# Optimization experiments

Hardware: AMD Instinct MI355X
Metric: run time of the kernel (lower is better)

The kernel has to match this reference:

```python
import jax, jax.numpy as jnp
import numpy as np

B, S, H, L, HEADS, VOCAB, POS = 32, 240, 1024, 8, 16, 48, 240
D = H // HEADS


def setup_inputs() -> dict:
    key = jax.random.key(0)
    ks = jax.random.split(key, 20)
    p = lambda k, shape: jax.random.normal(k, shape, jnp.float32) * 0.02
    x = jax.random.normal(ks[0], (B, S, VOCAB), jnp.float32)
    lengths = jnp.sort(jax.random.randint(ks[1], (B,), 120, S + 1))[::-1]
    lengths = lengths.at[0].set(S)  # padded max length == S
    return {
        "x": x,
        "w_emb": p(ks[2], (VOCAB, H)),
        "p_emb": p(ks[3], (POS, H)),
        "Wq": p(ks[4], (L, H, H)), "bq": p(ks[5], (L, H)),
        "Wk": p(ks[6], (L, H, H)), "bk": p(ks[7], (L, H)),
        "Wv": p(ks[8], (L, H, H)), "bv": p(ks[9], (L, H)),
        "W1": p(ks[10], (L, H, H)), "b1": p(ks[11], (L, H)),
        "W2": p(ks[12], (L, H, H)), "b2": p(ks[13], (L, H)),
        "ln1_s": jnp.ones((L, H), jnp.float32), "ln1_b": jnp.zeros((L, H), jnp.float32),
        "ln2_s": jnp.ones((L, H), jnp.float32), "ln2_b": jnp.zeros((L, H), jnp.float32),
        "Wfc": p(ks[14], (H, 4)), "bfc": p(ks[15], (4,)),
        "lengths": lengths,
    }


def _ln(x, s, b):
    m = jnp.mean(x, -1, keepdims=True)
    v = jnp.mean((x - m) ** 2, -1, keepdims=True)
    return (x - m) / jnp.sqrt(v + 1e-5) * s + b


def reference(x, w_emb, p_emb, Wq, bq, Wk, bk, Wv, bv, W1, b1, W2, b2,
              ln1_s, ln1_b, ln2_s, ln2_b, Wfc, bfc, lengths):
    tokens = jnp.argmax(x, -1)                      # [B,S] argmax over feature dim (48)
    valid = jnp.arange(S)[None, :] < lengths[:, None]  # [B,S] query-row validity
    # pack/unpack zeros out embeddings at padded positions; pos-enc added everywhere
    z = w_emb[tokens] * valid[..., None].astype(jnp.float32) + p_emb[None, :S]
    causal = jnp.tril(jnp.ones((S, S), bool))
    scale = 1.0 / jnp.sqrt(jnp.float32(H))          # source divides by sqrt(hidden), not sqrt(d_head)
    for i in range(L):
        q = (z @ Wq[i] + bq[i]).reshape(B, S, HEADS, D)
        k = (z @ Wk[i] + bk[i]).reshape(B, S, HEADS, D)
        v = (z @ Wv[i] + bv[i]).reshape(B, S, HEADS, D)
        scores = jnp.einsum('bqhd,bkhd->bhqk', q, k) * scale
        scores = jnp.where(causal, scores, -jnp.inf)
        # softmax over causal keys; padded query rows are zeroed (torch NaN->0 path)
        atten = jax.nn.softmax(scores, -1) * valid[:, None, :, None].astype(jnp.float32)
        out = jnp.einsum('bhqk,bkhd->bqhd', atten, v).reshape(B, S, H)
        z1 = _ln(z + out, ln1_s[i], ln1_b[i])       # dropout off in eval
        ff = jax.nn.gelu(z1 @ W1[i] + b1[i], approximate=False) @ W2[i] + b2[i]
        z = _ln(z1 + ff, ln2_s[i], ln2_b[i])
    z2 = jnp.mean(z, axis=1)                        # mean-pool includes padded positions (faithful)
    return jax.nn.softmax(z2 @ Wfc + bfc, axis=-1)
```

## Files before the change

### kernel.cpp

```cpp
#include <hip/hip_runtime.h>
#include <hip/hip_bf16.h>

#define Bz 32
#define Sz 240
#define Hz 1024
#define Lz 8
#define NHEADS 16
#define NVOCAB 48
#define DHEAD 64
#define VT_STRIDE 264

typedef unsigned short u16;
typedef unsigned int u32;
typedef __attribute__((ext_vector_type(8))) short short8v;
typedef __attribute__((ext_vector_type(4))) float floatx4;

__device__ __forceinline__ int get_len(const int* __restrict__ L, int b) {
  return (L[1] == 0) ? L[2 * b] : L[b];
}
__device__ __forceinline__ u16 f2bf(float f) {
  u32 u = __float_as_uint(f);
  return (u16)((u + 0x7FFFu + ((u >> 16) & 1u)) >> 16);
}
__device__ __forceinline__ float bf2f(u16 s) {
  return __uint_as_float(((u32)s) << 16);
}
__device__ __forceinline__ void async_copy16(const u16* g, u16* l) {
  __builtin_amdgcn_global_load_lds(
      (const __attribute__((address_space(1))) u32*)g,
      (__attribute__((address_space(3))) u32*)l, 16, 0, 0);
}

__global__ __launch_bounds__(256) void embed_kernel(
    const float* __restrict__ x, const float* __restrict__ w_emb,
    const float* __restrict__ p_emb, const int* __restrict__ lengths,
    float* __restrict__ z, u16* __restrict__ z_bf) {
  int bs = blockIdx.x;
  int b = bs / Sz, s = bs % Sz;
  __shared__ int stok;
  if (threadIdx.x == 0) {
    const float* xr = x + (size_t)bs * NVOCAB;
    float best = xr[0]; int bi = 0;
    for (int j = 1; j < NVOCAB; ++j) {
      float v = xr[j];
      if (v > best) { best = v; bi = j; }
    }
    stok = bi;
  }
  __syncthreads();
  int tok = stok;
  float valid = (s < get_len(lengths, b)) ? 1.f : 0.f;
  const float* we = w_emb + (size_t)tok * Hz;
  const float* pe = p_emb + (size_t)s * Hz;
  size_t base = (size_t)bs * Hz;
  for (int h = threadIdx.x; h < Hz; h += blockDim.x) {
    float v = we[h] * valid + pe[h];
    z[base + h] = v;
    z_bf[base + h] = f2bf(v);
  }
}

__global__ __launch_bounds__(256) void bias_concat(
    const float* __restrict__ bq, const float* __restrict__ bk,
    const float* __restrict__ bv, float* __restrict__ dst) {
  int i = blockIdx.x * 256 + threadIdx.x;
  int l = i / 3072, c = i % 3072;
  float v = (c < 1024) ? bq[l * 1024 + c]
          : (c < 2048) ? bk[l * 1024 + c - 1024]
                       : bv[l * 1024 + c - 2048];
  dst[i] = v;
}

struct WconvArgs { const float* src[5]; u16* dst[5]; };
__global__ __launch_bounds__(256) void wconv5(WconvArgs a) {
  __shared__ u16 T[32][33];
  const float* W = a.src[blockIdx.z];
  u16* wt = a.dst[blockIdx.z];
  int bi = blockIdx.y, bj = blockIdx.x;
  int r = threadIdx.x >> 3, c4 = (threadIdx.x & 7) * 4;
  float4 w4 = *(const float4*)(W + (size_t)(bi * 32 + r) * Hz + bj * 32 + c4);
  T[r][c4 + 0] = f2bf(w4.x); T[r][c4 + 1] = f2bf(w4.y);
  T[r][c4 + 2] = f2bf(w4.z); T[r][c4 + 3] = f2bf(w4.w);
  __syncthreads();
  u32 lo = (u32)T[c4 + 0][r] | ((u32)T[c4 + 1][r] << 16);
  u32 hi = (u32)T[c4 + 2][r] | ((u32)T[c4 + 3][r] << 16);
  uint2 val; val.x = lo; val.y = hi;
  *(uint2*)(wt + (size_t)(bj * 32 + r) * Hz + bi * 32 + c4) = val;
}

template <int BN, bool OUTBF16, bool GELU, bool RESID>
__global__ __launch_bounds__(512, 2) void gemm_mfma(
    const u16* __restrict__ A, const u16* __restrict__ Wt,
    const float* __restrict__ bias, const float* __restrict__ resid,
    void* __restrict__ Cv, int nco) {
  constexpr int MT = (BN == 256) ? 8 : 4;
  constexpr int WGC = (BN == 256) ? 4 : 2;
  constexpr int BKT = BN * 32;
  __shared__ u16 As[2][16384];
  __shared__ u16 Bs[2][BN * 64];
  int tid = threadIdx.x;
  int nwg = (int)gridDim.x;
  int id0 = blockIdx.x;
  int id = (id0 & 7) * (nwg >> 3) + (id0 >> 3);
  int ncols = nco / BN;
  int row0 = (id / ncols) * 256;
  int col0 = (id % ncols) * BN;

  int w = tid >> 6, lane = tid & 63;
  int l15 = lane & 15, lq = lane >> 4;
  int wr = w / WGC, wc = w % WGC;
  floatx4 acc[MT][4] = {};

  const u16* gA0 = A + (size_t)(row0 + 32 * w + l15) * 1024 + 8 * lq;
  const u16* gA1 = gA0 + 16 * 1024;
  const u16* gB0 = Wt + (size_t)(col0 + (BN == 256 ? 32 : 16) * w + l15) * 1024 + 8 * lq;
  const u16* gB1 = gB0 + 16 * 1024;

  auto stage = [&](int bb, int kk) {
#pragma unroll
    for (int kt = 0; kt < 2; ++kt) {
      async_copy16(gA0 + kk + 32 * kt, &As[bb][kt * 8192 + (2 * w) * 512]);
      async_copy16(gA1 + kk + 32 * kt, &As[bb][kt * 8192 + (2 * w + 1) * 512]);
      if constexpr (BN == 256) {
        async_copy16(gB0 + kk + 32 * kt, &Bs[bb][kt * BKT + (2 * w) * 512]);
        async_copy16(gB1 + kk + 32 * kt, &Bs[bb][kt * BKT + (2 * w + 1) * 512]);
      } else {
        async_copy16(gB0 + kk + 32 * kt, &Bs[bb][kt * BKT + w * 512]);
      }
    }
  };

  int afrag_off[MT], bfrag_off[4];
#pragma unroll
  for (int i = 0; i < MT; ++i)
    afrag_off[i] = (wr * MT + i) * 512 + lq * 128 + l15 * 8;
#pragma unroll
  for (int j = 0; j < 4; ++j)
    bfrag_off[j] = (wc * 4 + j) * 512 + lq * 128 + l15 * 8;

  stage(0, 0);
  stage(1, 64);
  if constexpr (BN == 256)
    __asm__ volatile("s_waitcnt vmcnt(8)" ::: "memory");
  else
    __asm__ volatile("s_waitcnt vmcnt(6)" ::: "memory");
  __builtin_amdgcn_s_barrier();
  __builtin_amdgcn_sched_barrier(0);

  int cur = 0;
  for (int k0 = 0; k0 < 1024; k0 += 64) {
    short8v af0[MT], bf0[4], af1[MT], bf1[4];
#pragma unroll
    for (int i = 0; i < MT; ++i) {
      af0[i] = *(const short8v*)(&As[cur][afrag_off[i]]);
      af1[i] = *(const short8v*)(&As[cur][8192 + afrag_off[i]]);
    }
#pragma unroll
    for (int j = 0; j < 4; ++j) {
      bf0[j] = *(const short8v*)(&Bs[cur][bfrag_off[j]]);
      bf1[j] = *(const short8v*)(&Bs[cur][BKT + bfrag_off[j]]);
    }
    __asm__ volatile("s_waitcnt lgkmcnt(0)" ::: "memory");
    __builtin_amdgcn_sched_barrier(0);
    __builtin_amdgcn_s_barrier();
    __builtin_amdgcn_sched_barrier(0);
    if (k0 + 128 < 1024) stage(cur, k0 + 128);
    __builtin_amdgcn_s_setprio(1);
#pragma unroll
    for (int mi = 0; mi < MT; ++mi)
#pragma unroll
      for (int ni = 0; ni < 4; ++ni)
        acc[mi][ni] = __builtin_amdgcn_mfma_f32_16x16x32_bf16(
            af0[mi], bf0[ni], acc[mi][ni], 0, 0, 0);
#pragma unroll
    for (int mi = 0; mi < MT; ++mi)
#pragma unroll
      for (int ni = 0; ni < 4; ++ni)
        acc[mi][ni] = __builtin_amdgcn_mfma_f32_16x16x32_bf16(
            af1[mi], bf1[ni], acc[mi][ni], 0, 0, 0);
    __builtin_amdgcn_s_setprio(0);
    if (k0 + 64 < 1024) {
      if (k0 + 128 < 1024) {
        if constexpr (BN == 256)
          __asm__ volatile("s_waitcnt vmcnt(8)" ::: "memory");
        else
          __asm__ volatile("s_waitcnt vmcnt(6)" ::: "memory");
      } else {
        __asm__ volatile("s_waitcnt vmcnt(0)" ::: "memory");
      }
      __builtin_amdgcn_s_barrier();
      __builtin_amdgcn_sched_barrier(0);
    }
    cur ^= 1;
  }

  int rowbase = row0 + wr * (MT * 16), colbase = col0 + wc * 64;
#pragma unroll
  for (int ni = 0; ni < 4; ++ni) {
    int col = colbase + ni * 16 + l15;
    float bcol = bias[col];
#pragma unroll
    for (int mi = 0; mi < MT; ++mi) {
      int rtop = rowbase + mi * 16 + lq * 4;
#pragma unroll
      for (int reg = 0; reg < 4; ++reg) {
        float vv = acc[mi][ni][reg] + bcol;
        if (RESID) vv += resid[(size_t)(rtop + reg) * nco + col];
        if (GELU) vv = 0.5f * vv * (1.f + erff(vv * 0.70710678118654752f));
        if (OUTBF16)
          ((u16*)Cv)[(size_t)(rtop + reg) * nco + col] = f2bf(vv);
        else
          ((float*)Cv)[(size_t)(rtop + reg) * nco + col] = vv;
      }
    }
  }
}

__global__ __launch_bounds__(256) void attention_kernel(
    const u16* __restrict__ qkv, const int* __restrict__ lengths,
    const float* __restrict__ zres, float* __restrict__ out) {
  const int LDQ = 3072;
  __shared__ u16 Vt[64 * VT_STRIDE];
  __shared__ u16 Pb[4][16 * 40];
  int hh = blockIdx.x & 1;
  int h = (blockIdx.x >> 1) & 15;
  int b = blockIdx.x >> 5;
  int tid = threadIdx.x;
  const size_t base = ((size_t)b * Sz) * LDQ + (size_t)h * DHEAD;
  const u16* qp = qkv + base;
  const u16* kp = qkv + base + 1024;
  const u16* vp = qkv + base + 2048;

  for (int idx = tid; idx < 256 * 16; idx += 256) {
    int key = idx >> 4, d4 = (idx & 15) * 4;
    uint2 vv;
    if (key < Sz) vv = *(const uint2*)(vp + (size_t)key * LDQ + d4);
    else { vv.x = 0u; vv.y = 0u; }
    Vt[(d4 + 0) * VT_STRIDE + key] = (u16)(vv.x & 0xFFFF);
    Vt[(d4 + 1) * VT_STRIDE + key] = (u16)(vv.x >> 16);
    Vt[(d4 + 2) * VT_STRIDE + key] = (u16)(vv.y & 0xFFFF);
    Vt[(d4 + 3) * VT_STRIDE + key] = (u16)(vv.y >> 16);
  }
  __syncthreads();

  int w = tid >> 6, lane = tid & 63;
  int qgroup = lane >> 4, qcol = lane & 15;
  int len_b = get_len(lengths, b);

  for (int qt = hh * 8 + w; qt < hh * 8 + 8 && qt < 15; qt += 4) {
    const u16* qrow = qp + (size_t)(qt * 16 + qcol) * LDQ;
    short8v aq0 = *(const short8v*)(qrow + qgroup * 8);
    short8v aq1 = *(const short8v*)(qrow + 32 + qgroup * 8);
    floatx4 o0 = {0.f, 0.f, 0.f, 0.f}, o1 = o0, o2 = o0, o3 = o0;
    float m_run[4] = {-1e30f, -1e30f, -1e30f, -1e30f};
    float l_run[4] = {0.f, 0.f, 0.f, 0.f};
    int nsteps = (qt + 2) >> 1;

    for (int st = 0; st < nsteps; ++st) {
      int t0 = 2 * st, t1 = 2 * st + 1;
      bool has1 = (t1 <= qt);
      floatx4 s0 = {0.f, 0.f, 0.f, 0.f};
      {
        const u16* kr = kp + (size_t)(t0 * 16 + qcol) * LDQ;
        short8v bk0 = *(const short8v*)(kr + qgroup * 8);
        short8v bk1 = *(const short8v*)(kr + 32 + qgroup * 8);
        s0 = __builtin_amdgcn_mfma_f32_16x16x32_bf16(aq0, bk0, s0, 0, 0, 0);
        s0 = __builtin_amdgcn_mfma_f32_16x16x32_bf16(aq1, bk1, s0, 0, 0, 0);
      }
      floatx4 s1 = {0.f, 0.f, 0.f, 0.f};
      if (has1) {
        const u16* kr = kp + (size_t)(t1 * 16 + qcol) * LDQ;
        short8v bk0 = *(const short8v*)(kr + qgroup * 8);
        short8v bk1 = *(const short8v*)(kr + 32 + qgroup * 8);
        s1 = __builtin_amdgcn_mfma_f32_16x16x32_bf16(aq0, bk0, s1, 0, 0, 0);
        s1 = __builtin_amdgcn_mfma_f32_16x16x32_bf16(aq1, bk1, s1, 0, 0, 0);
      }
      int kg0 = t0 * 16 + qcol, kg1 = t1 * 16 + qcol;
      float p0[4], p1[4];
#pragma unroll
      for (int rg = 0; rg < 4; ++rg) {
        int row_g = qt * 16 + qgroup * 4 + rg;
        float x0 = (kg0 <= row_g) ? s0[rg] * 0.03125f : -1e30f;
        float x1 = (has1 && kg1 <= row_g) ? s1[rg] * 0.03125f : -1e30f;
        float mx = fmaxf(x0, x1);
        mx = fmaxf(mx, __shfl_xor(mx, 1));
        mx = fmaxf(mx, __shfl_xor(mx, 2));
        mx = fmaxf(mx, __shfl_xor(mx, 4));
        mx = fmaxf(mx, __shfl_xor(mx, 8));
        float mnew = fmaxf(m_run[rg], mx);
        float alpha = __expf(m_run[rg] - mnew);
        float e0 = __expf(x0 - mnew);
        float e1 = __expf(x1 - mnew);
        float rs = e0 + e1;
        rs += __shfl_xor(rs, 1);
        rs += __shfl_xor(rs, 2);
        rs += __shfl_xor(rs, 4);
        rs += __shfl_xor(rs, 8);
        l_run[rg] = l_run[rg] * alpha + rs;
        m_run[rg] = mnew;
        o0[rg] *= alpha; o1[rg] *= alpha; o2[rg] *= alpha; o3[rg] *= alpha;
        p0[rg] = e0; p1[rg] = e1;
      }
#pragma unroll
      for (int rg = 0; rg < 4; ++rg) {
        int rl = qgroup * 4 + rg;
        Pb[w][rl * 40 + qcol] = f2bf(p0[rg]);
        Pb[w][rl * 40 + 16 + qcol] = f2bf(p1[rg]);
      }
      __asm__ volatile("s_waitcnt lgkmcnt(0)" ::: "memory");
      short8v pa = *(const short8v*)(&Pb[w][qcol * 40 + qgroup * 8]);
      int kb0 = st * 32 + qgroup * 8;
      short8v bv0 = *(const short8v*)(&Vt[(0 * 16 + qcol) * VT_STRIDE + kb0]);
      short8v bv1 = *(const short8v*)(&Vt[(1 * 16 + qcol) * VT_STRIDE + kb0]);
      short8v bv2 = *(const short8v*)(&Vt[(2 * 16 + qcol) * VT_STRIDE + kb0]);
      short8v bv3 = *(const short8v*)(&Vt[(3 * 16 + qcol) * VT_STRIDE + kb0]);
      o0 = __builtin_amdgcn_mfma_f32_16x16x32_bf16(pa, bv0, o0, 0, 0, 0);
      o1 = __builtin_amdgcn_mfma_f32_16x16x32_bf16(pa, bv1, o1, 0, 0, 0);
      o2 = __builtin_amdgcn_mfma_f32_16x16x32_bf16(pa, bv2, o2, 0, 0, 0);
      o3 = __builtin_amdgcn_mfma_f32_16x16x32_bf16(pa, bv3, o3, 0, 0, 0);
    }

#pragma unroll
    for (int rg = 0; rg < 4; ++rg) {
      int row_g = qt * 16 + qgroup * 4 + rg;
      float vmask = (row_g < len_b) ? (1.f / l_run[rg]) : 0.f;
      size_t ob = ((size_t)b * Sz + row_g) * Hz + (size_t)h * DHEAD + qcol;
      out[ob]      = zres[ob]      + o0[rg] * vmask;
      out[ob + 16] = zres[ob + 16] + o1[rg] * vmask;
      out[ob + 32] = zres[ob + 32] + o2[rg] * vmask;
      out[ob + 48] = zres[ob + 48] + o3[rg] * vmask;
    }
  }
}

__global__ __launch_bounds__(256) void add_ln_kernel(
    float* __restrict__ z, u16* __restrict__ z_bf, const float* __restrict__ r,
    const float* __restrict__ gamma, const float* __restrict__ beta) {
  int bs = blockIdx.x, tid = threadIdx.x;
  size_t base = (size_t)bs * Hz;
  __shared__ float sred[256];
  float4 v4 = *(const float4*)(r + base + tid * 4);
  float sum = v4.x + v4.y + v4.z + v4.w;
  sred[tid] = sum; __syncthreads();
  for (int off = 128; off > 0; off >>= 1) {
    if (tid < off) sred[tid] += sred[tid + off];
    __syncthreads();
  }
  float mean = sred[0] * (1.f / Hz); __syncthreads();
  float dx = v4.x - mean, dy = v4.y - mean, dz = v4.z - mean, dw = v4.w - mean;
  sred[tid] = dx * dx + dy * dy + dz * dz + dw * dw; __syncthreads();
  for (int off = 128; off > 0; off >>= 1) {
    if (tid < off) sred[tid] += sred[tid + off];
    __syncthreads();
  }
  float rstd = rsqrtf(sred[0] * (1.f / Hz) + 1e-5f);
  float4 g4 = *(const float4*)(gamma + tid * 4);
  float4 b4 = *(const float4*)(beta + tid * 4);
  float4 o;
  o.x = dx * rstd * g4.x + b4.x;
  o.y = dy * rstd * g4.y + b4.y;
  o.z = dz * rstd * g4.z + b4.z;
  o.w = dw * rstd * g4.w + b4.w;
  *(float4*)(z + base + tid * 4) = o;
  uint2 pk;
  pk.x = (u32)f2bf(o.x) | ((u32)f2bf(o.y) << 16);
  pk.y = (u32)f2bf(o.z) | ((u32)f2bf(o.w) << 16);
  *(uint2*)(z_bf + base + tid * 4) = pk;
}

__global__ __launch_bounds__(256) void pool1_kernel(
    const float* __restrict__ z, float* __restrict__ pooled) {
  int chunk = blockIdx.x, b = blockIdx.y, tid = threadIdx.x;
  int h = chunk * 128 + (tid & 127);
  int half = tid >> 7;
  __shared__ float sred[256];
  const float* zp = z + ((size_t)b * Sz + half * 120) * Hz + h;
  float s = 0.f;
  for (int i = 0; i < 120; ++i) s += zp[(size_t)i * Hz];
  sred[tid] = s; __syncthreads();
  if (tid < 128)
    pooled[(size_t)b * Hz + chunk * 128 + tid] =
        (sred[tid] + sred[tid + 128]) * (1.f / Sz);
}

__global__ __launch_bounds__(256) void pool2_kernel(
    const float* __restrict__ pooled, const float* __restrict__ Wfc,
    const float* __restrict__ bfc, float* __restrict__ out) {
  int b = blockIdx.x, tid = threadIdx.x;
  __shared__ float red[256][4];
  float acc[4] = {0.f, 0.f, 0.f, 0.f};
#pragma unroll
  for (int j = 0; j < 4; ++j) {
    int hh = tid * 4 + j;
    float z2 = pooled[(size_t)b * Hz + hh];
#pragma unroll
    for (int c = 0; c < 4; ++c) acc[c] += z2 * Wfc[hh * 4 + c];
  }
#pragma unroll
  for (int c = 0; c < 4; ++c) red[tid][c] = acc[c];
  __syncthreads();
  for (int off = 128; off > 0; off >>= 1) {
    if (tid < off)
#pragma unroll
      for (int c = 0; c < 4; ++c) red[tid][c] += red[tid + off][c];
    __syncthreads();
  }
  if (tid == 0) {
    float lg[4], m = -1e30f;
#pragma unroll
    for (int c = 0; c < 4; ++c) { lg[c] = red[0][c] + bfc[c]; m = fmaxf(m, lg[c]); }
    float s = 0.f;
#pragma unroll
    for (int c = 0; c < 4; ++c) { lg[c] = expf(lg[c] - m); s += lg[c]; }
    float inv = 1.f / s;
#pragma unroll
    for (int c = 0; c < 4; ++c) out[b * 4 + c] = lg[c] * inv;
  }
}

extern "C" void kernel_launch(void* const* d_in, const int* in_sizes, int n_in,
                              void* d_out, int out_size, void* d_ws, size_t ws_size,
                              hipStream_t stream) {
  const float* x     = (const float*)d_in[0];
  const float* w_emb = (const float*)d_in[1];
  const float* p_emb = (const float*)d_in[2];
  const float* Wq = (const float*)d_in[3];
  const float* bq = (const float*)d_in[4];
  const float* Wk = (const float*)d_in[5];
  const float* bk = (const float*)d_in[6];
  const float* Wv = (const float*)d_in[7];
  const float* bv = (const float*)d_in[8];
  const float* W1 = (const float*)d_in[9];
  const float* b1 = (const float*)d_in[10];
  const float* W2 = (const float*)d_in[11];
  const float* b2 = (const float*)d_in[12];
  const float* ln1s = (const float*)d_in[13];
  const float* ln1b = (const float*)d_in[14];
  const float* ln2s = (const float*)d_in[15];
  const float* ln2b = (const float*)d_in[16];
  const float* Wfc  = (const float*)d_in[17];
  const float* bfc  = (const float*)d_in[18];
  const int* lengths = (const int*)d_in[19];
  float* out = (float*)d_out;

  const size_t BSH = (size_t)Bz * Sz * Hz;
  float* z    = (float*)d_ws;
  float* ao   = z + BSH;
  u16* z_bf   = (u16*)(ao + BSH);
  u16* ffb    = z_bf + BSH;
  u16* qkv    = ffb + BSH;
  u16* wt     = qkv + 3 * BSH;
  float* bqkv = (float*)(wt + 5 * 1024 * 1024);
  float* pooled = bqkv + Lz * 3072;

  embed_kernel<<<Bz * Sz, 256, 0, stream>>>(x, w_emb, p_emb, lengths, z, z_bf);
  bias_concat<<<Lz * 3072 / 256, 256, 0, stream>>>(bq, bk, bv, bqkv);

  for (int i = 0; i < Lz; ++i) {
    size_t wo = (size_t)i * Hz * Hz, bo = (size_t)i * Hz;
    WconvArgs wa;
    wa.src[0] = Wq + wo; wa.src[1] = Wk + wo; wa.src[2] = Wv + wo;
    wa.src[3] = W1 + wo; wa.src[4] = W2 + wo;
    wa.dst[0] = wt;                     wa.dst[1] = wt + 1024 * 1024;
    wa.dst[2] = wt + 2 * 1024 * 1024;   wa.dst[3] = wt + 3 * 1024 * 1024;
    wa.dst[4] = wt + 4 * 1024 * 1024;
    wconv5<<<dim3(32, 32, 5), 256, 0, stream>>>(wa);

    gemm_mfma<256, true, false, false><<<30 * 12, 512, 0, stream>>>(
        z_bf, wt, bqkv + (size_t)i * 3072, nullptr, qkv, 3072);
    attention_kernel<<<Bz * NHEADS * 2, 256, 0, stream>>>(qkv, lengths, z, ao);
    add_ln_kernel<<<Bz * Sz, 256, 0, stream>>>(z, z_bf, ao, ln1s + bo, ln1b + bo);
    gemm_mfma<128, true, true, false><<<30 * 8, 512, 0, stream>>>(
        z_bf, wt + 3 * 1024 * 1024, b1 + bo, nullptr, ffb, 1024);
    gemm_mfma<128, false, false, true><<<30 * 8, 512, 0, stream>>>(
        ffb, wt + 4 * 1024 * 1024, b2 + bo, z, ao, 1024);
    add_ln_kernel<<<Bz * Sz, 256, 0, stream>>>(z, z_bf, ao, ln2s + bo, ln2b + bo);
  }
  pool1_kernel<<<dim3(8, Bz), 256, 0, stream>>>(z, pooled);
  pool2_kernel<<<Bz, 256, 0, stream>>>(pooled, Wfc, bfc, out);
}
```

Measured before the change: 2.170 ms.

## Use 192-wide QKV GEMM tiles and split LDS fragment loads per k-half

Generalizes the MFMA GEMM so it can use BN=192, with a new B-tile staging scheme, and switches the QKV projection to 192-column tiles. This raises the grid from 360 to 480 workgroups, giving better occupancy and wave balance across the CUs. The k-loop is also restructured: the second half-k fragments are loaded from LDS while the first MFMA batch runs, overlapping LDS reads with compute. In exchange each workgroup reuses its A tile over fewer columns, and the vmcnt wait counts change with the new copy layout.

```diff
diff --git a/kernel.cpp b/kernel.cpp
--- a/kernel.cpp
+++ b/kernel.cpp
@@ -93,9 +93,12 @@
     const u16* __restrict__ A, const u16* __restrict__ Wt,
     const float* __restrict__ bias, const float* __restrict__ resid,
     void* __restrict__ Cv, int nco) {
-  constexpr int MT = (BN == 256) ? 8 : 4;
-  constexpr int WGC = (BN == 256) ? 4 : 2;
-  constexpr int BKT = BN * 32;
+  constexpr int WGC = (BN == 192) ? 4 : 2;
+  constexpr int NT = BN / (WGC * 16);
+  constexpr int MT = (WGC == 4) ? 8 : 4;
+  constexpr int NB = (BN / 16) * 2 / 8;
+  constexpr int VM = 4 + NB;
+  constexpr int BST = BN * 32;
   __shared__ u16 As[2][16384];
   __shared__ u16 Bs[2][BN * 64];
   int tid = threadIdx.x;
@@ -109,82 +112,94 @@
   int w = tid >> 6, lane = tid & 63;
   int l15 = lane & 15, lq = lane >> 4;
   int wr = w / WGC, wc = w % WGC;
-  floatx4 acc[MT][4] = {};
+  floatx4 acc[MT][NT] = {};
 
   const u16* gA0 = A + (size_t)(row0 + 32 * w + l15) * 1024 + 8 * lq;
   const u16* gA1 = gA0 + 16 * 1024;
-  const u16* gB0 = Wt + (size_t)(col0 + (BN == 256 ? 32 : 16) * w + l15) * 1024 + 8 * lq;
-  const u16* gB1 = gB0 + 16 * 1024;
+  const u16* gBu[NB];
+  int bdst[NB];
+#pragma unroll
+  for (int i = 0; i < NB; ++i) {
+    int u = w + 8 * i;
+    int ktu = u / (BN / 16), cbu = u % (BN / 16);
+    gBu[i] = Wt + (size_t)(col0 + cbu * 16 + l15) * 1024 + ktu * 32 + 8 * lq;
+    bdst[i] = u * 512;
+  }
 
   auto stage = [&](int bb, int kk) {
 #pragma unroll
     for (int kt = 0; kt < 2; ++kt) {
       async_copy16(gA0 + kk + 32 * kt, &As[bb][kt * 8192 + (2 * w) * 512]);
       async_copy16(gA1 + kk + 32 * kt, &As[bb][kt * 8192 + (2 * w + 1) * 512]);
-      if constexpr (BN == 256) {
-        async_copy16(gB0 + kk + 32 * kt, &Bs[bb][kt * BKT + (2 * w) * 512]);
-        async_copy16(gB1 + kk + 32 * kt, &Bs[bb][kt * BKT + (2 * w + 1) * 512]);
-      } else {
-        async_copy16(gB0 + kk + 32 * kt, &Bs[bb][kt * BKT + w * 512]);
-      }
-    }
+    }
+#pragma unroll
+    for (int i = 0; i < NB; ++i)
+      async_copy16(gBu[i] + kk, &Bs[bb][bdst[i]]);
   };
 
-  int afrag_off[MT], bfrag_off[4];
+  int afrag_off[MT], bfrag_off[NT];
 #pragma unroll
   for (int i = 0; i < MT; ++i)
     afrag_off[i] = (wr * MT + i) * 512 + lq * 128 + l15 * 8;
 #pragma unroll
-  for (int j = 0; j < 4; ++j)
-    bfrag_off[j] = (wc * 4 + j) * 512 + lq * 128 + l15 * 8;
+  for (int j = 0; j < NT; ++j)
+    bfrag_off[j] = (wc * NT + j) * 512 + lq * 128 + l15 * 8;
+
+#define WAIT_VM_N()                                                  \
+  do {                                                               \
+    if constexpr (VM == 7)                                           \
+      __asm__ volatile("s_waitcnt vmcnt(7)" ::: "memory");           \
+    else                                                             \
+      __asm__ volatile("s_waitcnt vmcnt(6)" ::: "memory");           \
+  } while (0)
 
   stage(0, 0);
   stage(1, 64);
-  if constexpr (BN == 256)
-    __asm__ volatile("s_waitcnt vmcnt(8)" ::: "memory");
-  else
-    __asm__ volatile("s_waitcnt vmcnt(6)" ::: "memory");
+  WAIT_VM_N();
   __builtin_amdgcn_s_barrier();
   __builtin_amdgcn_sched_barrier(0);
 
   int cur = 0;
   for (int k0 = 0; k0 < 1024; k0 += 64) {
-    short8v af0[MT], bf0[4], af1[MT], bf1[4];
-#pragma unroll
-    for (int i = 0; i < MT; ++i) {
+    short8v af0[MT], bf0[NT], af1[MT], bf1[NT];
+#pragma unroll
+    for (int i = 0; i < MT; ++i)
       af0[i] = *(const short8v*)(&As[cur][afrag_off[i]]);
+#pragma unroll
+    for (int j = 0; j < NT; ++j)
+      bf0[j] = *(const short8v*)(&Bs[cur][bfrag_off[j]]);
+    __asm__ volatile("s_waitcnt lgkmcnt(0)" ::: "memory");
+    __builtin_amdgcn_sched_barrier(0);
+#pragma unroll
+    for (int i = 0; i < MT; ++i)
       af1[i] = *(const short8v*)(&As[cur][8192 + afrag_off[i]]);
-    }
-#pragma unroll
-    for (int j = 0; j < 4; ++j) {
-      bf0[j] = *(const short8v*)(&Bs[cur][bfrag_off[j]]);
-      bf1[j] = *(const short8v*)(&Bs[cur][BKT + bfrag_off[j]]);
-    }
+#pragma unroll
+    for (int j = 0; j < NT; ++j)
+      bf1[j] = *(const short8v*)(&Bs[cur][BST + bfrag_off[j]]);
+    __builtin_amdgcn_sched_barrier(0);
+    __builtin_amdgcn_s_setprio(1);
+#pragma unroll
+    for (int mi = 0; mi < MT; ++mi)
+#pragma unroll
+      for (int ni = 0; ni < NT; ++ni)
+        acc[mi][ni] = __builtin_amdgcn_mfma_f32_16x16x32_bf16(
+            af0[mi], bf0[ni], acc[mi][ni], 0, 0, 0);
+    __builtin_amdgcn_s_setprio(0);
     __asm__ volatile("s_waitcnt lgkmcnt(0)" ::: "memory");
     __builtin_amdgcn_sched_barrier(0);
     __builtin_amdgcn_s_barrier();
-    __builtin_amdgcn_sched_barrier(0);
     if (k0 + 128 < 1024) stage(cur, k0 + 128);
     __builtin_amdgcn_s_setprio(1);
 #pragma unroll
     for (int mi = 0; mi < MT; ++mi)
 #pragma unroll
-      for (int ni = 0; ni < 4; ++ni)
-        acc[mi][ni] = __builtin_amdgcn_mfma_f32_16x16x32_bf16(
-            af0[mi], bf0[ni], acc[mi][ni], 0, 0, 0);
-#pragma unroll
-    for (int mi = 0; mi < MT; ++mi)
-#pragma unroll
-      for (int ni = 0; ni < 4; ++ni)
+      for (int ni = 0; ni < NT; ++ni)
         acc[mi][ni] = __builtin_amdgcn_mfma_f32_16x16x32_bf16(
             af1[mi], bf1[ni], acc[mi][ni], 0, 0, 0);
     __builtin_amdgcn_s_setprio(0);
     if (k0 + 64 < 1024) {
       if (k0 + 128 < 1024) {
-        if constexpr (BN == 256)
-          __asm__ volatile("s_waitcnt vmcnt(8)" ::: "memory");
-        else
-          __asm__ volatile("s_waitcnt vmcnt(6)" ::: "memory");
+        WAIT_VM_N();
       } else {
         __asm__ volatile("s_waitcnt vmcnt(0)" ::: "memory");
       }
@@ -193,10 +208,11 @@
     }
     cur ^= 1;
   }
-
-  int rowbase = row0 + wr * (MT * 16), colbase = col0 + wc * 64;
-#pragma unroll
-  for (int ni = 0; ni < 4; ++ni) {
+#undef WAIT_VM_N
+
+  int rowbase = row0 + wr * (MT * 16), colbase = col0 + wc * (NT * 16);
+#pragma unroll
+  for (int ni = 0; ni < NT; ++ni) {
     int col = colbase + ni * 16 + l15;
     float bcol = bias[col];
 #pragma unroll
@@ -466,7 +482,7 @@
     wa.dst[4] = wt + 4 * 1024 * 1024;
     wconv5<<<dim3(32, 32, 5), 256, 0, stream>>>(wa);
 
-    gemm_mfma<256, true, false, false><<<30 * 12, 512, 0, stream>>>(
+    gemm_mfma<192, true, false, false><<<30 * 16, 512, 0, stream>>>(
         z_bf, wt, bqkv + (size_t)i * 3072, nullptr, qkv, 3072);
     attention_kernel<<<Bz * NHEADS * 2, 256, 0, stream>>>(qkv, lengths, z, ao);
     add_ln_kernel<<<Bz * Sz, 256, 0, stream>>>(z, z_bf, ao, ln1s + bo, ln1b + bo);
```

New measurement: 2.151 ms. Within noise of the previous version (-0.9%).
